# Performance work log

Measured on AMD Instinct MI355X. Metric: run time of the kernel, lower is better.

The kernel has to match this reference:

```python
import jax, jax.numpy as jnp
import numpy as np

N_NODES = 163840
N_EDGES = 2621440
F_IN = 64
F_HID = 64
SUBG = 20  # size_subgraph_samples
NEG_SLOPE = 0.2


def gat_conv(x, src, dst, W, a_src, a_dst, b):
    """PyG GATConv, heads=1, concat. src/dst already include self-loops."""
    n = x.shape[0]
    h = x @ W                               # [N, H]
    al_s = h @ a_src                        # [N]
    al_d = h @ a_dst                        # [N]
    e = jax.nn.leaky_relu(al_s[src] + al_d[dst], NEG_SLOPE)  # [E]
    # softmax over incoming edges of each dst node
    m = jax.ops.segment_max(e, dst, num_segments=n)
    ex = jnp.exp(e - m[dst])
    denom = jax.ops.segment_sum(ex, dst, num_segments=n)
    alpha = ex / (denom[dst] + 1e-16)
    msg = h[src] * alpha[:, None]           # [E, H]
    out = jax.ops.segment_sum(msg, dst, num_segments=n)
    return out + b


def setup_inputs() -> dict:
    key = jax.random.key(0)
    ks = jax.random.split(key, 12)
    s = 0.05
    return {
        "x": jax.random.normal(ks[0], (N_NODES, F_IN), jnp.float32),
        "edge_index": jax.random.randint(ks[1], (2, N_EDGES), 0, N_NODES, jnp.int64 if jax.config.jax_enable_x64 else jnp.int32),
        "W1": jax.random.normal(ks[2], (F_IN, F_HID), jnp.float32) * s,
        "a_src1": jax.random.normal(ks[3], (F_HID,), jnp.float32) * s,
        "a_dst1": jax.random.normal(ks[4], (F_HID,), jnp.float32) * s,
        "b1": jnp.zeros((F_HID,), jnp.float32),
        "W2": jax.random.normal(ks[5], (F_HID, F_HID), jnp.float32) * s,
        "a_src2": jax.random.normal(ks[6], (F_HID,), jnp.float32) * s,
        "a_dst2": jax.random.normal(ks[7], (F_HID,), jnp.float32) * s,
        "b2": jnp.zeros((F_HID,), jnp.float32),
        "W_out": jax.random.normal(ks[8], (F_HID * SUBG, 1), jnp.float32) * s,
        "b_out": jnp.zeros((1,), jnp.float32),
    }


def reference(x, edge_index, W1, a_src1, a_dst1, b1, W2, a_src2, a_dst2, b2, W_out, b_out):
    n = x.shape[0]
    loop = jnp.arange(n, dtype=edge_index.dtype)
    src = jnp.concatenate([edge_index[0], loop])  # add_self_loops=True
    dst = jnp.concatenate([edge_index[1], loop])
    h = gat_conv(x, src, dst, W1, a_src1, a_dst1, b1)
    h = jax.nn.relu(h)  # dropout is identity in eval mode
    h = gat_conv(h, src, dst, W2, a_src2, a_dst2, b2)
    h = jax.nn.relu(h)
    h = h.reshape(n // SUBG, F_HID * SUBG)
    return h @ W_out + b_out
```

## Files before the change

kernel.cpp:

```cpp
#include <hip/hip_runtime.h>
#include <math.h>

#define F 64
#define NPB 160
#define BCAP 3584

typedef __attribute__((ext_vector_type(8))) short bf16x8;
typedef __attribute__((ext_vector_type(4))) float f32x4;

__device__ inline unsigned short f2bf(float f) {
  unsigned int u = __float_as_uint(f);
  u += 0x7fffu + ((u >> 16) & 1u);
  return (unsigned short)(u >> 16);
}

__global__ __launch_bounds__(256) void k_prep(const float* __restrict__ W1, const float* __restrict__ W2,
                                              uint4* __restrict__ wf, int* __restrict__ bcnt, int nb,
                                              float* __restrict__ out, const float* __restrict__ bo, int ng,
                                              int* __restrict__ ssrc, int e) {
  int tid = threadIdx.x;
  if (blockIdx.x == 0) {
    for (int i = tid; i < 1024; i += 256) {
      int layer = i >> 9, rem = i & 511;
      int cb = rem >> 6, lane = rem & 63;
      int c = cb >> 1, kk = cb & 1;
      int l15 = lane & 15, quad = lane >> 4;
      const float* W = layer ? W2 : W1;
      unsigned short p[8];
      #pragma unroll
      for (int j = 0; j < 8; j++) {
        int kd = kk * 32 + quad * 8 + j;
        p[j] = f2bf(W[kd * F + c * 16 + l15]);
      }
      wf[i] = *(const uint4*)p;
    }
  } else {
    for (int i = tid; i < nb * 16; i += 256) bcnt[i] = 0;
    float b0 = bo[0];
    for (int i = tid; i < ng; i += 256) out[i] = b0;
    if (tid < 64) ssrc[e + tid] = 0;
  }
}

__device__ __forceinline__ void gemm_body(const float* __restrict__ in, const uint4* __restrict__ wf,
                                          const float* __restrict__ avs, const float* __restrict__ avd,
                                          unsigned short* __restrict__ hgb, float* __restrict__ als,
                                          float* __restrict__ ald, int n, int bid, int nbl) {
  int tid = threadIdx.x, lane = tid & 63, wv = tid >> 6;
  int l15 = lane & 15, quad = lane >> 4;
  bf16x8 bfr[4][2];
  #pragma unroll
  for (int cb = 0; cb < 8; cb++) {
    uint4 u = wf[cb * 64 + lane];
    bfr[cb >> 1][cb & 1] = *(const bf16x8*)&u;
  }
  float as_l[4], ad_l[4];
  #pragma unroll
  for (int c = 0; c < 4; c++) { as_l[c] = avs[c * 16 + l15]; ad_l[c] = avd[c * 16 + l15]; }

  int nchunks = n >> 6;
  for (int chunk = bid; chunk < nchunks; chunk += nbl) {
    int r0 = (chunk << 6) + (wv << 4);
    bf16x8 a0, a1;
    const float4* xr = (const float4*)(in + (size_t)(r0 + l15) * F + quad * 8);
    float4 xa = xr[0], xb = xr[1];
    float4 xc = xr[8], xd = xr[9];
    a0[0] = (short)f2bf(xa.x); a0[1] = (short)f2bf(xa.y); a0[2] = (short)f2bf(xa.z); a0[3] = (short)f2bf(xa.w);
    a0[4] = (short)f2bf(xb.x); a0[5] = (short)f2bf(xb.y); a0[6] = (short)f2bf(xb.z); a0[7] = (short)f2bf(xb.w);
    a1[0] = (short)f2bf(xc.x); a1[1] = (short)f2bf(xc.y); a1[2] = (short)f2bf(xc.z); a1[3] = (short)f2bf(xc.w);
    a1[4] = (short)f2bf(xd.x); a1[5] = (short)f2bf(xd.y); a1[6] = (short)f2bf(xd.z); a1[7] = (short)f2bf(xd.w);
    f32x4 cfr[4];
    #pragma unroll
    for (int c = 0; c < 4; c++) {
      cfr[c] = (f32x4){0.f, 0.f, 0.f, 0.f};
      cfr[c] = __builtin_amdgcn_mfma_f32_16x16x32_bf16(a0, bfr[c][0], cfr[c], 0, 0, 0);
      cfr[c] = __builtin_amdgcn_mfma_f32_16x16x32_bf16(a1, bfr[c][1], cfr[c], 0, 0, 0);
    }
    #pragma unroll
    for (int i = 0; i < 4; i++) {
      int row = r0 + quad * 4 + i;
      #pragma unroll
      for (int c = 0; c < 4; c++) hgb[(size_t)row * F + c * 16 + l15] = f2bf(cfr[c][i]);
      float ps = cfr[0][i] * as_l[0] + cfr[1][i] * as_l[1] + cfr[2][i] * as_l[2] + cfr[3][i] * as_l[3];
      float pd = cfr[0][i] * ad_l[0] + cfr[1][i] * ad_l[1] + cfr[2][i] * ad_l[2] + cfr[3][i] * ad_l[3];
      #pragma unroll
      for (int o = 1; o <= 8; o <<= 1) { ps += __shfl_xor(ps, o); pd += __shfl_xor(pd, o); }
      if (l15 == 0) { als[row] = ps; ald[row] = pd; }
    }
  }
}

__global__ __launch_bounds__(256) void k_scatter_gemm1(const int* __restrict__ esrc, const int* __restrict__ edst,
                                                       int* __restrict__ bcnt, unsigned int* __restrict__ binned,
                                                       int e, int ch, int S,
                                                       const float* __restrict__ x, const uint4* __restrict__ wf,
                                                       const float* __restrict__ avs, const float* __restrict__ avd,
                                                       unsigned short* __restrict__ hgb, float* __restrict__ als,
                                                       float* __restrict__ ald, int n) {
  int k = blockIdx.x, tid = threadIdx.x;
  if (k < S) {
    __shared__ int hist[1024];
    __shared__ int cur[1024];
    for (int i = tid; i < 1024; i += 256) hist[i] = 0;
    __syncthreads();
    int beg = k * ch, end = min(e, beg + ch);
    int len = end - beg;
    if (len <= 0) return;
    int nv = len >> 2;
    for (int g = tid; g < nv; g += 256) {
      int4 d4 = *(const int4*)(edst + beg + (g << 2));
      atomicAdd(&hist[d4.x / NPB], 1);
      atomicAdd(&hist[d4.y / NPB], 1);
      atomicAdd(&hist[d4.z / NPB], 1);
      atomicAdd(&hist[d4.w / NPB], 1);
    }
    for (int i = beg + (nv << 2) + tid; i < end; i += 256) atomicAdd(&hist[edst[i] / NPB], 1);
    __syncthreads();
    for (int b = tid; b < 1024; b += 256) {
      int c = hist[b];
      int base = 0;
      if (c) base = atomicAdd(&bcnt[b * 16], c);
      cur[b] = b * BCAP + base;
    }
    __syncthreads();
    for (int g = tid; g < nv; g += 256) {
      int i = beg + (g << 2);
      int4 d4 = *(const int4*)(edst + i);
      int4 s4 = *(const int4*)(esrc + i);
      #pragma unroll
      for (int j = 0; j < 4; j++) {
        int d = (j == 0) ? d4.x : (j == 1) ? d4.y : (j == 2) ? d4.z : d4.w;
        int s = (j == 0) ? s4.x : (j == 1) ? s4.y : (j == 2) ? s4.z : s4.w;
        int b = d / NPB;
        int p = atomicAdd(&cur[b], 1);
        if (p < (b + 1) * BCAP) binned[p] = (unsigned int)s | ((unsigned int)(d - b * NPB) << 24);
      }
    }
    for (int i = beg + (nv << 2) + tid; i < end; i += 256) {
      int d = edst[i];
      int b = d / NPB;
      int p = atomicAdd(&cur[b], 1);
      if (p < (b + 1) * BCAP) binned[p] = (unsigned int)esrc[i] | ((unsigned int)(d - b * NPB) << 24);
    }
    return;
  }
  gemm_body(x, wf, avs, avd, hgb, als, ald, n, k - S, (int)gridDim.x - S);
}

__global__ __launch_bounds__(256) void k_bucket_csr(const unsigned int* __restrict__ binned,
                                                    const int* __restrict__ bcnt,
                                                    int* __restrict__ ssrc, int* __restrict__ offs,
                                                    int n, int nb) {
  __shared__ int ncnt[NPB];
  __shared__ int cur[NPB];
  __shared__ int red[256];
  __shared__ int wsum[4];
  __shared__ int stage[BCAP];
  int b = blockIdx.x, tid = threadIdx.x;
  int lane = tid & 63, wv = tid >> 6;
  int acc = 0;
  for (int j = tid; j < b; j += 256) acc += min(bcnt[j * 16], BCAP);
  red[tid] = acc;
  __syncthreads();
  #pragma unroll
  for (int o = 128; o > 0; o >>= 1) {
    if (tid < o) red[tid] += red[tid + o];
    __syncthreads();
  }
  int outbase = red[0];
  int ecnt = min(bcnt[b * 16], BCAP);
  int node0 = b * NPB;
  int nn = min(NPB, n - node0);
  const uint4* bq = (const uint4*)(binned + (size_t)b * BCAP);
  int nv4 = ecnt >> 2;
  for (int i = tid; i < NPB; i += 256) ncnt[i] = 0;
  __syncthreads();
  for (int i = tid; i < nv4; i += 256) {
    uint4 q = bq[i];
    atomicAdd(&ncnt[q.x >> 24], 1);
    atomicAdd(&ncnt[q.y >> 24], 1);
    atomicAdd(&ncnt[q.z >> 24], 1);
    atomicAdd(&ncnt[q.w >> 24], 1);
  }
  for (int i = (nv4 << 2) + tid; i < ecnt; i += 256)
    atomicAdd(&ncnt[binned[(size_t)b * BCAP + i] >> 24], 1);
  __syncthreads();
  int v = (tid < nn) ? ncnt[tid] : 0;
  int x = v;
  #pragma unroll
  for (int o = 1; o <= 32; o <<= 1) { int y = __shfl_up(x, o); if (lane >= o) x += y; }
  if (lane == 63) wsum[wv] = x;
  __syncthreads();
  int add = 0;
  for (int w = 0; w < wv; w++) add += wsum[w];
  int incl = x + add;
  if (tid < nn) {
    int noff = incl - v;
    cur[tid] = noff;
    offs[node0 + tid] = outbase + noff;
  }
  __syncthreads();
  for (int i = tid; i < nv4; i += 256) {
    uint4 q = bq[i];
    int p0 = atomicAdd(&cur[q.x >> 24], 1); stage[p0] = (int)(q.x & 0xFFFFFFu);
    int p1 = atomicAdd(&cur[q.y >> 24], 1); stage[p1] = (int)(q.y & 0xFFFFFFu);
    int p2 = atomicAdd(&cur[q.z >> 24], 1); stage[p2] = (int)(q.z & 0xFFFFFFu);
    int p3 = atomicAdd(&cur[q.w >> 24], 1); stage[p3] = (int)(q.w & 0xFFFFFFu);
  }
  for (int i = (nv4 << 2) + tid; i < ecnt; i += 256) {
    unsigned int q = binned[(size_t)b * BCAP + i];
    int p = atomicAdd(&cur[q >> 24], 1);
    stage[p] = (int)(q & 0xFFFFFFu);
  }
  __syncthreads();
  for (int i = tid; i < ecnt; i += 256) ssrc[outbase + i] = stage[i];
  if (b == nb - 1 && tid == 0) offs[n] = outbase + ecnt;
}

__device__ __forceinline__ void agg_node(int node, int n, const int* __restrict__ offs,
                                         const int* __restrict__ ssrc,
                                         const uint4* __restrict__ hg4,
                                         const float* __restrict__ als,
                                         const float* __restrict__ ald,
                                         float4 bl0, float4 bl1, int l8, float r[8]) {
  int cnode = min(node, n - 1);
  int beg = offs[cnode];
  int deg = offs[cnode + 1] - beg;
  int degc = max(deg - 1, 0);
  if (deg == 0) beg = 0;
  float aldv = ald[cnode];

  float ts = als[cnode] + aldv;
  ts = fmaxf(ts, 0.2f * ts);
  float exs = __expf(ts);
  float s = exs;
  uint4 us = hg4[(size_t)cnode * 8 + l8];
  float acc[8];
  acc[0] = exs * __uint_as_float(us.x << 16);
  acc[1] = exs * __uint_as_float(us.x & 0xffff0000u);
  acc[2] = exs * __uint_as_float(us.y << 16);
  acc[3] = exs * __uint_as_float(us.y & 0xffff0000u);
  acc[4] = exs * __uint_as_float(us.z << 16);
  acc[5] = exs * __uint_as_float(us.z & 0xffff0000u);
  acc[6] = exs * __uint_as_float(us.w << 16);
  acc[7] = exs * __uint_as_float(us.w & 0xffff0000u);

  int dm = deg;
  #pragma unroll
  for (int o = 8; o <= 32; o <<= 1) dm = max(dm, __shfl_xor(dm, o));

  #pragma unroll 4
  for (int j = 0; j < dm; j++) {
    int jj = min(j, degc);
    int src = ssrc[beg + jj];
    float t = als[src] + aldv;
    t = fmaxf(t, 0.2f * t);
    float ex = (j < deg) ? __expf(t) : 0.f;
    s += ex;
    uint4 u = hg4[(size_t)src * 8 + l8];
    acc[0] = fmaf(ex, __uint_as_float(u.x << 16), acc[0]);
    acc[1] = fmaf(ex, __uint_as_float(u.x & 0xffff0000u), acc[1]);
    acc[2] = fmaf(ex, __uint_as_float(u.y << 16), acc[2]);
    acc[3] = fmaf(ex, __uint_as_float(u.y & 0xffff0000u), acc[3]);
    acc[4] = fmaf(ex, __uint_as_float(u.z << 16), acc[4]);
    acc[5] = fmaf(ex, __uint_as_float(u.z & 0xffff0000u), acc[5]);
    acc[6] = fmaf(ex, __uint_as_float(u.w << 16), acc[6]);
    acc[7] = fmaf(ex, __uint_as_float(u.w & 0xffff0000u), acc[7]);
  }

  float iv = 1.f / (s + 1e-16f);
  r[0] = fmaxf(fmaf(acc[0], iv, bl0.x), 0.f);
  r[1] = fmaxf(fmaf(acc[1], iv, bl0.y), 0.f);
  r[2] = fmaxf(fmaf(acc[2], iv, bl0.z), 0.f);
  r[3] = fmaxf(fmaf(acc[3], iv, bl0.w), 0.f);
  r[4] = fmaxf(fmaf(acc[4], iv, bl1.x), 0.f);
  r[5] = fmaxf(fmaf(acc[5], iv, bl1.y), 0.f);
  r[6] = fmaxf(fmaf(acc[6], iv, bl1.z), 0.f);
  r[7] = fmaxf(fmaf(acc[7], iv, bl1.w), 0.f);
}

__global__ __launch_bounds__(256) void k_spmm_g2(const int* __restrict__ offs, const int* __restrict__ ssrc,
                                                 const unsigned short* __restrict__ hgb,
                                                 const float* __restrict__ als, const float* __restrict__ ald,
                                                 const float* __restrict__ bias, const uint4* __restrict__ wf2,
                                                 const float* __restrict__ avs, const float* __restrict__ avd,
                                                 unsigned short* __restrict__ hgb2, float* __restrict__ als2,
                                                 float* __restrict__ ald2, int n) {
  __shared__ __align__(16) unsigned short hsh[64][72];
  int tid = threadIdx.x, lane = tid & 63, wv = tid >> 6;
  int g8 = lane >> 3, l8 = lane & 7;
  const uint4* hg4 = (const uint4*)hgb;
  float4 bl0 = ((const float4*)bias)[l8 * 2];
  float4 bl1 = ((const float4*)bias)[l8 * 2 + 1];

  for (int p = 0; p < 2; p++) {
    int row = p * 32 + wv * 8 + g8;
    int node = blockIdx.x * 64 + row;
    float r[8];
    agg_node(node, n, offs, ssrc, hg4, als, ald, bl0, bl1, l8, r);
    unsigned short pk[8];
    #pragma unroll
    for (int k = 0; k < 8; k++) pk[k] = f2bf(r[k]);
    *(uint4*)&hsh[row][l8 * 8] = *(const uint4*)pk;
  }
  __syncthreads();

  int l15 = lane & 15, quad = lane >> 4;
  bf16x8 bfr[4][2];
  #pragma unroll
  for (int cb = 0; cb < 8; cb++) {
    uint4 u = wf2[cb * 64 + lane];
    bfr[cb >> 1][cb & 1] = *(const bf16x8*)&u;
  }
  float as_l[4], ad_l[4];
  #pragma unroll
  for (int c = 0; c < 4; c++) { as_l[c] = avs[c * 16 + l15]; ad_l[c] = avd[c * 16 + l15]; }

  int r0 = wv << 4;
  uint4 u0 = *(const uint4*)&hsh[r0 + l15][quad * 8];
  uint4 u1 = *(const uint4*)&hsh[r0 + l15][quad * 8 + 32];
  bf16x8 a0 = *(const bf16x8*)&u0;
  bf16x8 a1 = *(const bf16x8*)&u1;
  f32x4 cfr[4];
  #pragma unroll
  for (int c = 0; c < 4; c++) {
    cfr[c] = (f32x4){0.f, 0.f, 0.f, 0.f};
    cfr[c] = __builtin_amdgcn_mfma_f32_16x16x32_bf16(a0, bfr[c][0], cfr[c], 0, 0, 0);
    cfr[c] = __builtin_amdgcn_mfma_f32_16x16x32_bf16(a1, bfr[c][1], cfr[c], 0, 0, 0);
  }
  #pragma unroll
  for (int i = 0; i < 4; i++) {
    int row = blockIdx.x * 64 + r0 + quad * 4 + i;
    #pragma unroll
    for (int c = 0; c < 4; c++) hgb2[(size_t)row * F + c * 16 + l15] = f2bf(cfr[c][i]);
    float ps = cfr[0][i] * as_l[0] + cfr[1][i] * as_l[1] + cfr[2][i] * as_l[2] + cfr[3][i] * as_l[3];
    float pd = cfr[0][i] * ad_l[0] + cfr[1][i] * ad_l[1] + cfr[2][i] * ad_l[2] + cfr[3][i] * ad_l[3];
    #pragma unroll
    for (int o = 1; o <= 8; o <<= 1) { ps += __shfl_xor(ps, o); pd += __shfl_xor(pd, o); }
    if (l15 == 0) { als2[row] = ps; ald2[row] = pd; }
  }
}

__global__ __launch_bounds__(256) void k_spmm_out(const int* __restrict__ offs, const int* __restrict__ ssrc,
                                                  const unsigned short* __restrict__ hgb,
                                                  const float* __restrict__ als, const float* __restrict__ ald,
                                                  const float* __restrict__ bias, const float* __restrict__ Wout,
                                                  float* __restrict__ out, int n) {
  int tid = threadIdx.x, lane = tid & 63, wv = tid >> 6;
  int g8 = lane >> 3, l8 = lane & 7;
  const uint4* hg4 = (const uint4*)hgb;
  float4 bl0 = ((const float4*)bias)[l8 * 2];
  float4 bl1 = ((const float4*)bias)[l8 * 2 + 1];

  __shared__ float gsl[3];
  if (tid < 3) gsl[tid] = 0.f;

  int node = (blockIdx.x * 4 + wv) * 8 + g8;
  bool nodeok = node < n;
  int cnode = min(node, n - 1);
  float r[8];
  agg_node(node, n, offs, ssrc, hg4, als, ald, bl0, bl1, l8, r);

  int node0 = blockIdx.x * 32;
  int grp0 = node0 / 20;
  int grp = cnode / 20, slot = cnode - grp * 20;
  const float* wr = Wout + slot * F + l8 * 8;
  float dot = 0.f;
  #pragma unroll
  for (int k = 0; k < 8; k++) dot = fmaf(r[k], wr[k], dot);
  #pragma unroll
  for (int o = 1; o <= 4; o <<= 1) dot += __shfl_xor(dot, o);
  __syncthreads();
  if (nodeok && l8 == 0) atomicAdd(&gsl[grp - grp0], dot);
  __syncthreads();
  if (tid < 3) {
    float v = gsl[tid];
    if (v != 0.f) atomicAdd(out + grp0 + tid, v);
  }
}

extern "C" void kernel_launch(void* const* d_in, const int* in_sizes, int n_in,
                              void* d_out, int out_size, void* d_ws, size_t ws_size,
                              hipStream_t stream) {
  const float* x   = (const float*)d_in[0];
  const int*   ei  = (const int*)d_in[1];
  const float* W1  = (const float*)d_in[2];
  const float* as1 = (const float*)d_in[3];
  const float* ad1 = (const float*)d_in[4];
  const float* b1  = (const float*)d_in[5];
  const float* W2  = (const float*)d_in[6];
  const float* as2 = (const float*)d_in[7];
  const float* ad2 = (const float*)d_in[8];
  const float* b2  = (const float*)d_in[9];
  const float* Wo  = (const float*)d_in[10];
  const float* bo  = (const float*)d_in[11];
  float* out = (float*)d_out;

  const int N = in_sizes[0] / F;
  const int E = in_sizes[1] / 2;
  const int* esrc = ei;
  const int* edst = ei + E;

  size_t off = 0;
  auto alloc = [&](size_t bytes) -> void* {
    void* p = (char*)d_ws + off;
    off += (bytes + 255) & ~(size_t)255;
    return p;
  };
  unsigned short* hgb  = (unsigned short*)alloc((size_t)N * F * 2);
  unsigned short* hgb2 = (unsigned short*)alloc((size_t)N * F * 2);
  float* als  = (float*)alloc((size_t)N * 4);
  float* ald  = (float*)alloc((size_t)N * 4);
  float* als2 = (float*)alloc((size_t)N * 4);
  float* ald2 = (float*)alloc((size_t)N * 4);
  int* offs   = (int*)alloc((size_t)(N + 1) * 4);
  int* bcnt   = (int*)alloc((size_t)1024 * 16 * 4);
  int* ssrc   = (int*)alloc((size_t)(E + 64) * 4);
  unsigned int* binned = (unsigned int*)alloc((size_t)1024 * BCAP * 4);
  uint4* wf   = (uint4*)alloc(16384);
  (void)ws_size; (void)n_in; (void)out_size;

  const int NG = N / 20;
  const int NB = (N + NPB - 1) / NPB;
  const int S = 256;
  const int CH = (((E + S - 1) / S) + 3) & ~3;

  k_prep<<<2, 256, 0, stream>>>(W1, W2, wf, bcnt, NB, out, bo, NG, ssrc, E);
  k_scatter_gemm1<<<S + (N >> 6), 256, 0, stream>>>(esrc, edst, bcnt, binned, E, CH, S,
                                                    x, wf, as1, ad1, hgb, als, ald, N);
  k_bucket_csr<<<NB, 256, 0, stream>>>(binned, bcnt, ssrc, offs, N, NB);
  k_spmm_g2<<<(N >> 6), 256, 0, stream>>>(offs, ssrc, hgb, als, ald, b1, wf + 512, as2, ad2,
                                          hgb2, als2, ald2, N);
  k_spmm_out<<<(N >> 5), 256, 0, stream>>>(offs, ssrc, hgb2, als2, ald2, b2, Wo, out, N);
}
```

Measured before the change: 273.4 us.

## Pad per-node CSR to 4-aligned fixed-stride buckets and vectorize index loads

Each bucket now writes its edge list to a fixed-stride region of ssrc, which removes the per-block prefix reduction over all earlier bucket counts. Every node's edge list is padded to a multiple of four, and the degree is stored in a new ndeg array. This lets the aggregation loop fetch four source indices per uint4 load. The binned scratch buffer reuses the hgb2 allocation, which is safe only because hgb2 is written after bucket_csr. The cost is extra zero-initialisation of shared memory and padded gathers of node 0 for the pad slots, which are masked out.

```diff
diff --git a/kernel.cpp b/kernel.cpp
--- a/kernel.cpp
+++ b/kernel.cpp
@@ -4,6 +4,8 @@
 #define F 64
 #define NPB 160
 #define BCAP 3584
+#define SSTRIDE 4096
+#define STAGE_N 4096
 
 typedef __attribute__((ext_vector_type(8))) short bf16x8;
 typedef __attribute__((ext_vector_type(4))) float f32x4;
@@ -17,7 +19,7 @@
 __global__ __launch_bounds__(256) void k_prep(const float* __restrict__ W1, const float* __restrict__ W2,
                                               uint4* __restrict__ wf, int* __restrict__ bcnt, int nb,
                                               float* __restrict__ out, const float* __restrict__ bo, int ng,
-                                              int* __restrict__ ssrc, int e) {
+                                              int* __restrict__ ssrc) {
   int tid = threadIdx.x;
   if (blockIdx.x == 0) {
     for (int i = tid; i < 1024; i += 256) {
@@ -38,7 +40,7 @@
     for (int i = tid; i < nb * 16; i += 256) bcnt[i] = 0;
     float b0 = bo[0];
     for (int i = tid; i < ng; i += 256) out[i] = b0;
-    if (tid < 64) ssrc[e + tid] = 0;
+    if (tid < 64) ssrc[tid] = 0;
   }
 }
 
@@ -150,31 +152,22 @@
 __global__ __launch_bounds__(256) void k_bucket_csr(const unsigned int* __restrict__ binned,
                                                     const int* __restrict__ bcnt,
                                                     int* __restrict__ ssrc, int* __restrict__ offs,
-                                                    int n, int nb) {
+                                                    int* __restrict__ ndeg, int n) {
   __shared__ int ncnt[NPB];
   __shared__ int cur[NPB];
-  __shared__ int red[256];
   __shared__ int wsum[4];
-  __shared__ int stage[BCAP];
+  __shared__ int ptot_sh;
+  __shared__ int stage[STAGE_N];
   int b = blockIdx.x, tid = threadIdx.x;
   int lane = tid & 63, wv = tid >> 6;
-  int acc = 0;
-  for (int j = tid; j < b; j += 256) acc += min(bcnt[j * 16], BCAP);
-  red[tid] = acc;
-  __syncthreads();
-  #pragma unroll
-  for (int o = 128; o > 0; o >>= 1) {
-    if (tid < o) red[tid] += red[tid + o];
-    __syncthreads();
-  }
-  int outbase = red[0];
   int ecnt = min(bcnt[b * 16], BCAP);
   int node0 = b * NPB;
   int nn = min(NPB, n - node0);
+  for (int i = tid; i < NPB; i += 256) ncnt[i] = 0;
+  for (int i = tid; i < STAGE_N; i += 256) stage[i] = 0;
+  __syncthreads();
   const uint4* bq = (const uint4*)(binned + (size_t)b * BCAP);
   int nv4 = ecnt >> 2;
-  for (int i = tid; i < NPB; i += 256) ncnt[i] = 0;
-  __syncthreads();
   for (int i = tid; i < nv4; i += 256) {
     uint4 q = bq[i];
     atomicAdd(&ncnt[q.x >> 24], 1);
@@ -185,7 +178,7 @@
   for (int i = (nv4 << 2) + tid; i < ecnt; i += 256)
     atomicAdd(&ncnt[binned[(size_t)b * BCAP + i] >> 24], 1);
   __syncthreads();
-  int v = (tid < nn) ? ncnt[tid] : 0;
+  int v = (tid < nn) ? ((ncnt[tid] + 3) & ~3) : 0;
   int x = v;
   #pragma unroll
   for (int o = 1; o <= 32; o <<= 1) { int y = __shfl_up(x, o); if (lane >= o) x += y; }
@@ -197,7 +190,9 @@
   if (tid < nn) {
     int noff = incl - v;
     cur[tid] = noff;
-    offs[node0 + tid] = outbase + noff;
+    offs[node0 + tid] = b * SSTRIDE + noff;
+    ndeg[node0 + tid] = ncnt[tid];
+    if (tid == nn - 1) ptot_sh = incl;
   }
   __syncthreads();
   for (int i = tid; i < nv4; i += 256) {
@@ -213,21 +208,21 @@
     stage[p] = (int)(q & 0xFFFFFFu);
   }
   __syncthreads();
-  for (int i = tid; i < ecnt; i += 256) ssrc[outbase + i] = stage[i];
-  if (b == nb - 1 && tid == 0) offs[n] = outbase + ecnt;
+  int ptot = ptot_sh;
+  int* dst = ssrc + (size_t)b * SSTRIDE;
+  for (int i = tid; i < ptot; i += 256) dst[i] = stage[i];
 }
 
 __device__ __forceinline__ void agg_node(int node, int n, const int* __restrict__ offs,
+                                         const int* __restrict__ ndeg,
                                          const int* __restrict__ ssrc,
                                          const uint4* __restrict__ hg4,
                                          const float* __restrict__ als,
                                          const float* __restrict__ ald,
                                          float4 bl0, float4 bl1, int l8, float r[8]) {
   int cnode = min(node, n - 1);
-  int beg = offs[cnode];
-  int deg = offs[cnode + 1] - beg;
-  int degc = max(deg - 1, 0);
-  if (deg == 0) beg = 0;
+  int deg = ndeg[cnode];
+  int beg = (deg > 0) ? offs[cnode] : 0;
   float aldv = ald[cnode];
 
   float ts = als[cnode] + aldv;
@@ -248,24 +243,30 @@
   int dm = deg;
   #pragma unroll
   for (int o = 8; o <= 32; o <<= 1) dm = max(dm, __shfl_xor(dm, o));
-
-  #pragma unroll 4
-  for (int j = 0; j < dm; j++) {
-    int jj = min(j, degc);
-    int src = ssrc[beg + jj];
-    float t = als[src] + aldv;
-    t = fmaxf(t, 0.2f * t);
-    float ex = (j < deg) ? __expf(t) : 0.f;
-    s += ex;
-    uint4 u = hg4[(size_t)src * 8 + l8];
-    acc[0] = fmaf(ex, __uint_as_float(u.x << 16), acc[0]);
-    acc[1] = fmaf(ex, __uint_as_float(u.x & 0xffff0000u), acc[1]);
-    acc[2] = fmaf(ex, __uint_as_float(u.y << 16), acc[2]);
-    acc[3] = fmaf(ex, __uint_as_float(u.y & 0xffff0000u), acc[3]);
-    acc[4] = fmaf(ex, __uint_as_float(u.z << 16), acc[4]);
-    acc[5] = fmaf(ex, __uint_as_float(u.z & 0xffff0000u), acc[5]);
-    acc[6] = fmaf(ex, __uint_as_float(u.w << 16), acc[6]);
-    acc[7] = fmaf(ex, __uint_as_float(u.w & 0xffff0000u), acc[7]);
+  int dm4 = (dm + 3) >> 2;
+  int own4 = max((deg + 3) >> 2, 1);
+
+  const uint4* s4p = (const uint4*)(ssrc + beg);
+  for (int j4 = 0; j4 < dm4; j4++) {
+    uint4 s4 = s4p[min(j4, own4 - 1)];
+    int jb = j4 << 2;
+    #pragma unroll
+    for (int u = 0; u < 4; u++) {
+      int src = (u == 0) ? (int)s4.x : (u == 1) ? (int)s4.y : (u == 2) ? (int)s4.z : (int)s4.w;
+      float t = als[src] + aldv;
+      t = fmaxf(t, 0.2f * t);
+      float ex = (jb + u < deg) ? __expf(t) : 0.f;
+      s += ex;
+      uint4 uu = hg4[(size_t)src * 8 + l8];
+      acc[0] = fmaf(ex, __uint_as_float(uu.x << 16), acc[0]);
+      acc[1] = fmaf(ex, __uint_as_float(uu.x & 0xffff0000u), acc[1]);
+      acc[2] = fmaf(ex, __uint_as_float(uu.y << 16), acc[2]);
+      acc[3] = fmaf(ex, __uint_as_float(uu.y & 0xffff0000u), acc[3]);
+      acc[4] = fmaf(ex, __uint_as_float(uu.z << 16), acc[4]);
+      acc[5] = fmaf(ex, __uint_as_float(uu.z & 0xffff0000u), acc[5]);
+      acc[6] = fmaf(ex, __uint_as_float(uu.w << 16), acc[6]);
+      acc[7] = fmaf(ex, __uint_as_float(uu.w & 0xffff0000u), acc[7]);
+    }
   }
 
   float iv = 1.f / (s + 1e-16f);
@@ -279,7 +280,8 @@
   r[7] = fmaxf(fmaf(acc[7], iv, bl1.w), 0.f);
 }
 
-__global__ __launch_bounds__(256) void k_spmm_g2(const int* __restrict__ offs, const int* __restrict__ ssrc,
+__global__ __launch_bounds__(256) void k_spmm_g2(const int* __restrict__ offs, const int* __restrict__ ndeg,
+                                                 const int* __restrict__ ssrc,
                                                  const unsigned short* __restrict__ hgb,
                                                  const float* __restrict__ als, const float* __restrict__ ald,
                                                  const float* __restrict__ bias, const uint4* __restrict__ wf2,
@@ -297,7 +299,7 @@
     int row = p * 32 + wv * 8 + g8;
     int node = blockIdx.x * 64 + row;
     float r[8];
-    agg_node(node, n, offs, ssrc, hg4, als, ald, bl0, bl1, l8, r);
+    agg_node(node, n, offs, ndeg, ssrc, hg4, als, ald, bl0, bl1, l8, r);
     unsigned short pk[8];
     #pragma unroll
     for (int k = 0; k < 8; k++) pk[k] = f2bf(r[k]);
@@ -341,7 +343,8 @@
   }
 }
 
-__global__ __launch_bounds__(256) void k_spmm_out(const int* __restrict__ offs, const int* __restrict__ ssrc,
+__global__ __launch_bounds__(256) void k_spmm_out(const int* __restrict__ offs, const int* __restrict__ ndeg,
+                                                  const int* __restrict__ ssrc,
                                                   const unsigned short* __restrict__ hgb,
                                                   const float* __restrict__ als, const float* __restrict__ ald,
                                                   const float* __restrict__ bias, const float* __restrict__ Wout,
@@ -359,7 +362,7 @@
   bool nodeok = node < n;
   int cnode = min(node, n - 1);
   float r[8];
-  agg_node(node, n, offs, ssrc, hg4, als, ald, bl0, bl1, l8, r);
+  agg_node(node, n, offs, ndeg, ssrc, hg4, als, ald, bl0, bl1, l8, r);
 
   int node0 = blockIdx.x * 32;
   int grp0 = node0 / 20;
@@ -414,22 +417,24 @@
   float* als2 = (float*)alloc((size_t)N * 4);
   float* ald2 = (float*)alloc((size_t)N * 4);
   int* offs   = (int*)alloc((size_t)(N + 1) * 4);
+  int* ndeg   = (int*)alloc((size_t)N * 4);
   int* bcnt   = (int*)alloc((size_t)1024 * 16 * 4);
-  int* ssrc   = (int*)alloc((size_t)(E + 64) * 4);
-  unsigned int* binned = (unsigned int*)alloc((size_t)1024 * BCAP * 4);
+  int* ssrc   = (int*)alloc(((size_t)1024 * SSTRIDE) * 4);
   uint4* wf   = (uint4*)alloc(16384);
   (void)ws_size; (void)n_in; (void)out_size;
+
+  unsigned int* binned = (unsigned int*)hgb2;
 
   const int NG = N / 20;
   const int NB = (N + NPB - 1) / NPB;
   const int S = 256;
   const int CH = (((E + S - 1) / S) + 3) & ~3;
 
-  k_prep<<<2, 256, 0, stream>>>(W1, W2, wf, bcnt, NB, out, bo, NG, ssrc, E);
+  k_prep<<<2, 256, 0, stream>>>(W1, W2, wf, bcnt, NB, out, bo, NG, ssrc);
   k_scatter_gemm1<<<S + (N >> 6), 256, 0, stream>>>(esrc, edst, bcnt, binned, E, CH, S,
                                                     x, wf, as1, ad1, hgb, als, ald, N);
-  k_bucket_csr<<<NB, 256, 0, stream>>>(binned, bcnt, ssrc, offs, N, NB);
-  k_spmm_g2<<<(N >> 6), 256, 0, stream>>>(offs, ssrc, hgb, als, ald, b1, wf + 512, as2, ad2,
+  k_bucket_csr<<<NB, 256, 0, stream>>>(binned, bcnt, ssrc, offs, ndeg, N);
+  k_spmm_g2<<<(N >> 6), 256, 0, stream>>>(offs, ndeg, ssrc, hgb, als, ald, b1, wf + 512, as2, ad2,
                                           hgb2, als2, ald2, N);
-  k_spmm_out<<<(N >> 5), 256, 0, stream>>>(offs, ssrc, hgb2, als2, ald2, b2, Wo, out, N);
-}
+  k_spmm_out<<<(N >> 5), 256, 0, stream>>>(offs, ndeg, ssrc, hgb2, als2, ald2, b2, Wo, out, N);
+}
```

New measurement: 295.1 us. 1.08x slower.
